# Kernel tuning notes

Measured on AMD Instinct MI355X. Metric: run time of the kernel, lower is better.

The kernel has to match this reference:

```python
import jax, jax.numpy as jnp
import numpy as np

N_HEAD = 16
ROPE_BASE = 10000.0
EPS = 1e-6


def _rms_norm(x):
    return x / jnp.sqrt(jnp.mean(x * x, axis=-1, keepdims=True) + EPS)


def _rotary_cos_sin(n_pos, dim, dtype):
    # NOTE: faithful to the source, n_pos == n_head (not seq_len) because
    # Rotary.forward reads x.shape[2] of a (B,T,H,D) tensor.
    inv_freq = 1.0 / (ROPE_BASE ** (jnp.arange(0, dim, 2, dtype=jnp.float32) / dim))
    t = jnp.arange(n_pos, dtype=jnp.float32)
    freqs = jnp.outer(t, inv_freq)  # (n_pos, dim//2)
    return jnp.cos(freqs).astype(dtype)[None, None], jnp.sin(freqs).astype(dtype)[None, None]


def _apply_rotary(x, cos, sin):
    d = x.shape[-1] // 2
    x1, x2 = x[..., :d], x[..., d:]
    return jnp.concatenate([x1 * cos + x2 * sin, -x1 * sin + x2 * cos], axis=-1)


def setup_inputs() -> dict:
    key = jax.random.key(0)
    ks = jax.random.split(key, 8)
    B, T, C = 4, 1024, 2048
    x = jax.random.normal(ks[0], (B, T, C), dtype=jnp.float32)
    v1 = jax.random.normal(ks[1], (B, T, N_HEAD, C // N_HEAD), dtype=jnp.float32)
    s = 0.02
    W_qkv = jax.random.normal(ks[2], (C, 3 * C), dtype=jnp.float32) * s
    b_qkv = jax.random.normal(ks[3], (3 * C,), dtype=jnp.float32) * s
    W_proj = jax.random.normal(ks[4], (C, C), dtype=jnp.float32) * s
    b_proj = jax.random.normal(ks[5], (C,), dtype=jnp.float32) * s
    lamb = jnp.float32(0.5)
    return {"x": x, "v1": v1, "W_qkv": W_qkv, "b_qkv": b_qkv,
            "W_proj": W_proj, "b_proj": b_proj, "lamb": lamb}


def reference(x, v1, W_qkv, b_qkv, W_proj, b_proj, lamb):
    B, T, C = x.shape
    H = N_HEAD
    D = C // H
    qkv = x @ W_qkv + b_qkv  # (B,T,3C)
    q, k, v = jnp.split(qkv, 3, axis=-1)
    q = q.reshape(B, T, H, D)
    k = k.reshape(B, T, H, D)
    v = v.reshape(B, T, H, D)
    v1 = v1.reshape(B, T, H, D)
    value = (1.0 - lamb) * v + lamb * v1  # lambda value-residual mix
    q = _rms_norm(q)
    k = _rms_norm(k)
    cos, sin = _rotary_cos_sin(H, D, x.dtype)  # rotary over head axis (source bug, kept)
    q = _apply_rotary(q, cos, sin)
    k = _apply_rotary(k, cos, sin)
    # causal attention, default flex_attention scale 1/sqrt(D)
    scale = 1.0 / jnp.sqrt(jnp.float32(D)).astype(x.dtype)
    scores = jnp.einsum('bqhd,bkhd->bhqk', q, k) * scale
    causal = jnp.tril(jnp.ones((T, T), dtype=bool))
    scores = jnp.where(causal[None, None], scores, jnp.finfo(scores.dtype).min)
    probs = jax.nn.softmax(scores, axis=-1)
    attn = jnp.einsum('bhqk,bkhd->bqhd', probs, value).reshape(B, T, C)
    out = attn @ W_proj + b_proj
    return out, v1
```

## Files before the change

### kernel.cpp

```cpp
#include <hip/hip_runtime.h>
#include <stdint.h>
#include <stddef.h>

typedef unsigned short u16;
typedef __attribute__((ext_vector_type(8))) short  bf16x8;
typedef __attribute__((ext_vector_type(4))) unsigned short u16x4;
typedef __attribute__((ext_vector_type(4))) float  f32x4;

#define DEVI __device__ __forceinline__

DEVI float bf2f(u16 u){ union{uint32_t i; float f;} v; v.i = ((uint32_t)u)<<16; return v.f; }
DEVI u16 f2bf(float f){ union{float f; uint32_t i;} v; v.f=f; uint32_t r = v.i + 0x7fffu + ((v.i>>16)&1u); return (u16)(r>>16); }

DEVI void gload_lds16(const void* g, void* l){
  __builtin_amdgcn_global_load_lds((const __attribute__((address_space(1))) void*)g,
                                   (__attribute__((address_space(3))) void*)l, 16, 0, 0);
}

__global__ void k_cvt_bf16(const float* __restrict__ in, u16* __restrict__ out, int n){
  int i = (blockIdx.x*256 + threadIdx.x)*4;
  int st = gridDim.x*256*4;
  for (; i < n; i += st){
    f32x4 v = *(const f32x4*)(in + i);
    u16x4 o;
    #pragma unroll
    for (int j=0;j<4;j++) o[j] = f2bf(v[j]);
    *(u16x4*)(out + i) = o;
  }
}

__global__ __launch_bounds__(256) void k_transpose_cvt(const float* __restrict__ in, u16* __restrict__ out, int K, int N){
  __shared__ float tile[32][33];
  int nb = blockIdx.x*32, kb = blockIdx.y*32;
  int tx = threadIdx.x & 31, ty = threadIdx.x >> 5;
  #pragma unroll
  for (int i=0;i<32;i+=8)
    tile[ty+i][tx] = in[(size_t)(kb+ty+i)*N + nb+tx];
  __syncthreads();
  #pragma unroll
  for (int i=0;i<32;i+=8)
    out[(size_t)(nb+ty+i)*K + kb+tx] = f2bf(tile[tx][ty+i]);
}

#define STG(LP, GP, KH) \
  gload_lds16((GP) + offs[0] + (KH)*32, (LP) + (KH)*8192 + tid*8); \
  gload_lds16((GP) + offs[1] + (KH)*32, (LP) + (KH)*8192 + 4096 + tid*8);

#define RD_A(SP, KH, MH, DST) \
  { _Pragma("unroll") for (int f=0; f<4; f++){ \
      int row_ = wm*128 + (MH)*64 + f*16 + lr; \
      int rp_ = row_>>1; \
      int slot_ = ((((row_&1)<<2) | lg) ^ (rp_&7)); \
      DST[f] = *(const bf16x8*)((const char*)(SP) + (KH)*16384 + rp_*128 + slot_*16); } }

#define RD_B(SP, KH, DST) \
  { _Pragma("unroll") for (int nf=0; nf<4; nf++){ \
      int row_ = wn*64 + nf*16 + lr; \
      int rp_ = row_>>1; \
      int slot_ = ((((row_&1)<<2) | lg) ^ (rp_&7)); \
      DST[nf] = *(const bf16x8*)((const char*)(SP) + (KH)*16384 + rp_*128 + slot_*16); } }

#define MMQ(MH, AA, BB) \
  __builtin_amdgcn_s_setprio(1); \
  { _Pragma("unroll") for (int f=0; f<4; f++) \
    { _Pragma("unroll") for (int nf=0; nf<4; nf++) \
      acc[(MH)*4+f][nf] = __builtin_amdgcn_mfma_f32_16x16x32_bf16(AA[f], BB[nf], acc[(MH)*4+f][nf], 0,0,0); } } \
  __builtin_amdgcn_s_setprio(0);

#define BAR_LGKM \
  __builtin_amdgcn_s_barrier(); \
  __builtin_amdgcn_sched_barrier(0); \
  asm volatile("s_waitcnt lgkmcnt(0)" ::: "memory"); \
  __builtin_amdgcn_sched_barrier(0);

#define WAITV(N) asm volatile("s_waitcnt vmcnt(" #N ")" ::: "memory");
#define ORDER_FENCE __builtin_amdgcn_sched_barrier(0); asm volatile("" ::: "memory");

template<bool OUT_BF16>
__global__ __launch_bounds__(512) void k_gemm256(
    const u16* __restrict__ A, const u16* __restrict__ Bt,
    const float* __restrict__ bias, void* __restrict__ Cout,
    int M, int N, int K, int nbn)
{
  __shared__ __attribute__((aligned(16))) u16 sAm[2][2][8192];
  __shared__ __attribute__((aligned(16))) u16 sBm[2][2][8192];
  int nwg = gridDim.x;
  int orig = blockIdx.x;
  int wgid = (orig & 7)*(nwg>>3) + (orig>>3);
  int bm = wgid / nbn, bn = wgid % nbn;
  const int tid = threadIdx.x;
  const int wid = tid>>6, l = tid&63;
  const int lr = l&15, lg = l>>4;
  const int wm = wid>>2, wn = wid&3;
  const size_t rowA = (size_t)bm*256;
  const size_t rowB = (size_t)bn*256;

  uint32_t offs[2];
  #pragma unroll
  for (int it=0; it<2; it++){
    int cc = it*512 + tid;
    int rp = cc>>3, comb = (cc&7) ^ (rp&7);
    int row = rp*2 + (comb>>2), k16 = comb&3;
    offs[it] = (uint32_t)(row*K + k16*8);
  }
  const u16* Abase = A + rowA*K;
  const u16* Bbase = Bt + rowB*K;

  f32x4 acc[8][4] = {};
  bf16x8 a0[4], a1[4], b0[4], b1[4];
  const int NT = K>>6;

  STG(&sAm[0][0][0], Abase, 0);
  STG(&sBm[0][0][0], Bbase, 0);
  ORDER_FENCE;
  STG(&sAm[0][0][0], Abase, 1);
  STG(&sBm[0][0][0], Bbase, 1);
  WAITV(0);
  __builtin_amdgcn_s_barrier();
  __builtin_amdgcn_sched_barrier(0);

  const u16* An = Abase + 64;
  const u16* Bn = Bbase + 64;
  for (int kt=0; kt<NT-1; ++kt){
    const u16* sAr = &sAm[kt&1][0][0];
    const u16* sBr = &sBm[kt&1][0][0];
    u16* sAw = &sAm[(kt&1)^1][0][0];
    u16* sBw = &sBm[(kt&1)^1][0][0];
    RD_B(sBr, 0, b0);
    RD_A(sAr, 0, 0, a0);
    STG(sAw, An, 0);
    BAR_LGKM;
    MMQ(0, a0, b0);
    RD_A(sAr, 0, 1, a1);
    STG(sBw, Bn, 0);
    WAITV(4);
    BAR_LGKM;
    MMQ(1, a1, b0);
    RD_B(sBr, 1, b1);
    RD_A(sAr, 1, 0, a0);
    STG(sAw, An, 1);
    BAR_LGKM;
    MMQ(0, a0, b1);
    RD_A(sAr, 1, 1, a1);
    STG(sBw, Bn, 1);
    WAITV(4);
    BAR_LGKM;
    MMQ(1, a1, b1);
    An += 64; Bn += 64;
  }
  {
    const u16* sAr = &sAm[(NT-1)&1][0][0];
    const u16* sBr = &sBm[(NT-1)&1][0][0];
    RD_B(sBr, 0, b0);
    RD_A(sAr, 0, 0, a0);
    BAR_LGKM;
    MMQ(0, a0, b0);
    RD_A(sAr, 0, 1, a1);
    WAITV(0);
    BAR_LGKM;
    MMQ(1, a1, b0);
    RD_B(sBr, 1, b1);
    RD_A(sAr, 1, 0, a0);
    BAR_LGKM;
    MMQ(0, a0, b1);
    RD_A(sAr, 1, 1, a1);
    BAR_LGKM;
    MMQ(1, a1, b1);
  }

  #pragma unroll
  for (int nf=0; nf<4; nf++){
    int col = bn*256 + wn*64 + nf*16 + lr;
    float bv = bias[col];
    #pragma unroll
    for (int m=0; m<8; m++){
      #pragma unroll
      for (int j=0; j<4; j++){
        int row = bm*256 + wm*128 + m*16 + lg*4 + j;
        float v = acc[m][nf][j] + bv;
        if (OUT_BF16) ((u16*)Cout)[(size_t)row*N + col] = f2bf(v);
        else          ((float*)Cout)[(size_t)row*N + col] = v;
      }
    }
  }
}

template<bool OUT_BF16>
__global__ __launch_bounds__(256) void k_gemm_bt(
    const u16* __restrict__ A, const u16* __restrict__ Bt,
    const float* __restrict__ bias, void* __restrict__ Cout,
    int M, int N, int K, int nbn)
{
  __shared__ __attribute__((aligned(16))) u16 sA[128*64];
  __shared__ __attribute__((aligned(16))) u16 sB[128*64];
  int nwg = gridDim.x;
  int orig = blockIdx.x;
  int wgid = (orig & 7)*(nwg>>3) + (orig>>3);
  int bm = wgid / nbn, bn = wgid % nbn;
  const int tid = threadIdx.x;
  const int w = tid>>6, l = tid&63;
  const int lr = l&15, lg = l>>4;
  const int wr = (w>>1)*64, wc = (w&1)*64;
  const size_t rowA = (size_t)bm*128;
  const size_t rowB = (size_t)bn*128;
  f32x4 acc[4][4] = {};
  for (int k0=0; k0<K; k0+=64){
    #pragma unroll
    for (int it=0; it<4; ++it){
      int c = it*256 + tid;
      int r = c>>3, k8 = (c&7) ^ (r&7);
      gload_lds16(A + (rowA+r)*K + k0 + k8*8, &sA[c*8]);
    }
    #pragma unroll
    for (int it=0; it<4; ++it){
      int c = it*256 + tid;
      int r = c>>3, k8 = (c&7) ^ (r&7);
      gload_lds16(Bt + (rowB+r)*K + k0 + k8*8, &sB[c*8]);
    }
    __syncthreads();
    #pragma unroll
    for (int ks=0; ks<2; ++ks){
      bf16x8 af[4], bfr[4];
      #pragma unroll
      for (int m=0;m<4;m++){
        int row = wr + m*16 + lr, k = ks*32 + lg*8;
        int byt = ((row<<7) + (k<<1)) ^ ((row&7)<<4);
        af[m] = *(const bf16x8*)((const char*)sA + byt);
      }
      #pragma unroll
      for (int n=0;n<4;n++){
        int row = wc + n*16 + lr, k = ks*32 + lg*8;
        int byt = ((row<<7) + (k<<1)) ^ ((row&7)<<4);
        bfr[n] = *(const bf16x8*)((const char*)sB + byt);
      }
      #pragma unroll
      for (int m=0;m<4;m++)
        #pragma unroll
        for (int n=0;n<4;n++)
          acc[m][n] = __builtin_amdgcn_mfma_f32_16x16x32_bf16(af[m], bfr[n], acc[m][n], 0,0,0);
    }
    __syncthreads();
  }
  #pragma unroll
  for (int n=0;n<4;n++){
    int col = bn*128 + wc + n*16 + lr;
    float bv = bias[col];
    #pragma unroll
    for (int m=0;m<4;m++){
      #pragma unroll
      for (int j=0;j<4;j++){
        int row = bm*128 + wr + m*16 + lg*4 + j;
        float v = acc[m][n][j] + bv;
        if (OUT_BF16) ((u16*)Cout)[(size_t)row*N + col] = f2bf(v);
        else          ((float*)Cout)[(size_t)row*N + col] = v;
      }
    }
  }
}

DEVI void unpack16(const u16* p, float* f){
  bf16x8 a = *(const bf16x8*)p, b = *(const bf16x8*)(p+8);
  #pragma unroll
  for (int i=0;i<8;i++){ f[i]=bf2f((u16)a[i]); f[8+i]=bf2f((u16)b[i]); }
}

__global__ __launch_bounds__(256) void k_qkv_post(
    const u16*  __restrict__ qkv,
    const float* __restrict__ v1,
    const float* __restrict__ lambp,
    u16* __restrict__ qn,
    u16* __restrict__ kn,
    u16* __restrict__ vT,
    float* __restrict__ v1out)
{
  __shared__ float cosv[64], sinv[64];
  __shared__ __attribute__((aligned(16))) u16 sv[64][136];
  int bid = blockIdx.x;
  int tb = bid & 15, h = (bid>>4)&15, b = bid>>8;
  int tid = threadIdx.x;
  if (tid < 64){
    float ang = (float)h * exp2f(-(float)tid * 0.2076205059304595f);
    cosv[tid] = cosf(ang);
    sinv[tid] = sinf(ang);
  }
  float lamb = lambp[0];
  int row = tid>>2, p = tid&3;
  int t = tb*64 + row;
  size_t base = ((size_t)(b*1024 + t))*6144 + (size_t)h*128;
  __syncthreads();

  #pragma unroll
  for (int qc=0; qc<2; ++qc){
    const u16* src = qkv + base + qc*2048;
    u16* dst = (qc==0 ? qn : kn) + ((size_t)(b*1024+t))*2048 + h*128;
    int j0 = p*16;
    float x1[16], x2[16];
    unpack16(src + j0, x1);
    unpack16(src + 64 + j0, x2);
    float ss = 0.f;
    #pragma unroll
    for (int i=0;i<16;i++) ss += x1[i]*x1[i] + x2[i]*x2[i];
    ss += __shfl_xor(ss, 1);
    ss += __shfl_xor(ss, 2);
    float rn = rsqrtf(ss*(1.0f/128.0f) + 1e-6f);
    bf16x8 o1a,o1b,o2a,o2b;
    #pragma unroll
    for (int i=0;i<16;i++){
      float c = cosv[j0+i], s = sinv[j0+i];
      u16 a = f2bf(( x1[i]*c + x2[i]*s)*rn);
      u16 bq= f2bf((-x1[i]*s + x2[i]*c)*rn);
      if (i<8){ o1a[i]=(short)a; o2a[i]=(short)bq; } else { o1b[i-8]=(short)a; o2b[i-8]=(short)bq; }
    }
    *(bf16x8*)(dst + j0)      = o1a;
    *(bf16x8*)(dst + j0 + 8)  = o1b;
    *(bf16x8*)(dst + 64 + j0)     = o2a;
    *(bf16x8*)(dst + 64 + j0 + 8) = o2b;
  }

  {
    const u16* srcv = qkv + base + 4096;
    size_t v1off = (((size_t)(b*1024+t))*16 + h)*128;
    const float* src1 = v1 + v1off;
    float* dst1 = v1out + v1off;
    int d0 = p*32;
    #pragma unroll
    for (int c8=0;c8<4;c8++){
      bf16x8 vv = *(const bf16x8*)(srcv + d0 + c8*8);
      f32x4 a0 = *(const f32x4*)(src1 + d0 + c8*8);
      f32x4 a1 = *(const f32x4*)(src1 + d0 + c8*8 + 4);
      *(f32x4*)(dst1 + d0 + c8*8) = a0;
      *(f32x4*)(dst1 + d0 + c8*8 + 4) = a1;
      bf16x8 o;
      #pragma unroll
      for (int i=0;i<8;i++){
        float x1v = (i<4)? a0[i] : a1[i-4];
        o[i] = (short)f2bf((1.0f-lamb)*bf2f((u16)vv[i]) + lamb*x1v);
      }
      *(bf16x8*)(&sv[row][d0 + c8*8]) = o;
    }
  }
  __syncthreads();
  {
    int d = tid>>1, tc = (tid&1)*32;
    u16 tmp[32];
    #pragma unroll
    for (int i=0;i<32;i++) tmp[i] = sv[tc+i][d];
    u16* dst = vT + (((size_t)(b*16+h))*128 + d)*1024 + tb*64 + tc;
    #pragma unroll
    for (int c8=0;c8<4;c8++){
      bf16x8 o;
      #pragma unroll
      for (int i=0;i<8;i++) o[i]=(short)tmp[c8*8+i];
      *(bf16x8*)(dst + c8*8) = o;
    }
  }
}

__global__ __launch_bounds__(256) void k_attn(
    const u16* __restrict__ Q,
    const u16* __restrict__ Kn,
    const u16* __restrict__ Vt,
    u16* __restrict__ O)
{
  __shared__ __attribute__((aligned(16))) u16 sK[2][64*128];
  __shared__ __attribute__((aligned(16))) u16 sV[2][128*64];
  __shared__ __attribute__((aligned(16))) u16 sP[4][16*64];
  int bid = blockIdx.x;
  int qi = 15 - (bid>>6);
  int bh = bid & 63;
  int h = bh & 15, b = bh >> 4;
  int tid = threadIdx.x, w = tid>>6, l = tid&63, lr = l&15, lg = l>>4;
  int qrow = qi*64 + w*16;
  bf16x8 aq[4];
  {
    const u16* qp = Q + ((size_t)(b*1024 + qrow + lr))*2048 + h*128 + lg*8;
    #pragma unroll
    for (int ks=0; ks<4; ++ks) aq[ks] = *(const bf16x8*)(qp + ks*32);
  }
  f32x4 accO[8] = {};
  float mrun[4], srun[4];
  #pragma unroll
  for (int j=0;j<4;j++){ mrun[j] = -INFINITY; srun[j]=0.f; }
  const float scale = 0.08838834764831845f;
  const size_t kbase = (size_t)(b*1024)*2048 + (size_t)h*128;
  const u16* vbase = Vt + ((size_t)(b*16+h))*128*1024;

  auto STAGE = [&](int kt, int buf){
    #pragma unroll
    for (int it=0; it<4; ++it){
      int c = it*256+tid;
      int key = c>>4, d16 = (c&15)^(key&7);
      gload_lds16(Kn + kbase + (size_t)(kt*64+key)*2048 + d16*8, &sK[buf][c*8]);
    }
    #pragma unroll
    for (int it=0; it<4; ++it){
      int c = it*256+tid;
      int d = c>>3, k8 = (c&7)^(d&7);
      gload_lds16(vbase + (size_t)d*1024 + kt*64 + k8*8, &sV[buf][c*8]);
    }
  };

  STAGE(0, 0);
  int cur = 0;
  for (int kt=0; kt<=qi; ++kt){
    if (kt < qi){
      STAGE(kt+1, cur^1);
      asm volatile("s_waitcnt vmcnt(8)" ::: "memory");
    } else {
      asm volatile("s_waitcnt vmcnt(0)" ::: "memory");
    }
    __builtin_amdgcn_s_barrier();
    __builtin_amdgcn_sched_barrier(0);
    const char* kb = (const char*)sK[cur];
    const char* vb = (const char*)sV[cur];

    f32x4 accS[4] = {};
    __builtin_amdgcn_s_setprio(1);
    #pragma unroll
    for (int ks=0; ks<4; ++ks){
      #pragma unroll
      for (int n=0;n<4;n++){
        int key = n*16+lr, k = ks*32+lg*8;
        int byt = ((key<<8) + (k<<1)) ^ ((key&7)<<4);
        bf16x8 bk = *(const bf16x8*)(kb + byt);
        accS[n] = __builtin_amdgcn_mfma_f32_16x16x32_bf16(aq[ks], bk, accS[n], 0,0,0);
      }
    }
    __builtin_amdgcn_s_setprio(0);
    bool diag = (kt == qi);
    float pj[4][4];
    #pragma unroll
    for (int j=0;j<4;j++){
      int qg = qrow + lg*4 + j;
      float mx = -INFINITY;
      #pragma unroll
      for (int n=0;n<4;n++){
        float s = accS[n][j]*scale;
        if (diag && (kt*64 + n*16 + lr) > qg) s = -1e30f;
        pj[n][j] = s;
        mx = fmaxf(mx, s);
      }
      #pragma unroll
      for (int off=1; off<16; off<<=1) mx = fmaxf(mx, __shfl_xor(mx, off));
      float mnew = fmaxf(mrun[j], mx);
      float fac = __expf(mrun[j] - mnew);
      float ps = 0.f;
      #pragma unroll
      for (int n=0;n<4;n++){ float e = __expf(pj[n][j]-mnew); pj[n][j]=e; ps += e; }
      #pragma unroll
      for (int off=1; off<16; off<<=1) ps += __shfl_xor(ps, off);
      srun[j] = srun[j]*fac + ps;
      mrun[j] = mnew;
      #pragma unroll
      for (int n=0;n<8;n++) accO[n][j] *= fac;
    }
    #pragma unroll
    for (int n=0;n<4;n++)
      #pragma unroll
      for (int j=0;j<4;j++){
        int q = lg*4+j, key = n*16+lr;
        int byt = ((q<<7) + (key<<1)) ^ ((q&7)<<4);
        *(u16*)((char*)sP[w] + byt) = f2bf(pj[n][j]);
      }
    bf16x8 pA[2];
    #pragma unroll
    for (int ks=0; ks<2; ++ks){
      int k = ks*32 + lg*8;
      int byt = ((lr<<7) + (k<<1)) ^ ((lr&7)<<4);
      pA[ks] = *(const bf16x8*)((const char*)sP[w] + byt);
    }
    __builtin_amdgcn_s_setprio(1);
    #pragma unroll
    for (int ks=0; ks<2; ++ks)
      #pragma unroll
      for (int n=0;n<8;n++){
        int d = n*16+lr, k = ks*32+lg*8;
        int byt = ((d<<7) + (k<<1)) ^ ((d&7)<<4);
        bf16x8 bv = *(const bf16x8*)(vb + byt);
        accO[n] = __builtin_amdgcn_mfma_f32_16x16x32_bf16(pA[ks], bv, accO[n], 0,0,0);
      }
    __builtin_amdgcn_s_setprio(0);
    __builtin_amdgcn_s_barrier();
    cur ^= 1;
  }
  #pragma unroll
  for (int j=0;j<4;j++){
    float inv = 1.0f / srun[j];
    int row = qrow + lg*4 + j;
    u16* op = O + ((size_t)(b*1024+row))*2048 + h*128;
    #pragma unroll
    for (int n=0;n<8;n++)
      op[n*16+lr] = f2bf(accO[n][j]*inv);
  }
}

extern "C" void kernel_launch(void* const* d_in, const int* in_sizes, int n_in,
                              void* d_out, int out_size, void* d_ws, size_t ws_size,
                              hipStream_t stream)
{
  const float* x     = (const float*)d_in[0];
  const float* v1    = (const float*)d_in[1];
  const float* Wqkv  = (const float*)d_in[2];
  const float* bqkv  = (const float*)d_in[3];
  const float* Wproj = (const float*)d_in[4];
  const float* bproj = (const float*)d_in[5];
  const float* lamb  = (const float*)d_in[6];

  char* ws = (char*)d_ws;
  u16* qkv_b  = (u16*)(ws);
  u16* WqkvT  = (u16*)(ws +  50331648);
  u16* WprojT = (u16*)(ws +  75497472);
  u16* xb     = (u16*)(ws +  83886080);
  u16* vT     = xb;
  u16* qn     = (u16*)(ws + 100663296);
  u16* kn     = (u16*)(ws + 117440512);
  u16* attn_b = qkv_b;

  float* out = (float*)d_out;

  hipLaunchKernelGGL(k_cvt_bf16, dim3(2048), dim3(256), 0, stream, x, xb, 8388608);
  hipLaunchKernelGGL(k_transpose_cvt, dim3(192, 64), dim3(256), 0, stream, Wqkv,  WqkvT,  2048, 6144);
  hipLaunchKernelGGL(k_transpose_cvt, dim3(64, 64),  dim3(256), 0, stream, Wproj, WprojT, 2048, 2048);
  hipLaunchKernelGGL((k_gemm256<true>), dim3(384), dim3(512), 0, stream, xb, WqkvT, bqkv, (void*)qkv_b, 4096, 6144, 2048, 24);
  hipLaunchKernelGGL(k_qkv_post, dim3(1024), dim3(256), 0, stream, qkv_b, v1, lamb, qn, kn, vT, out + 8388608);
  hipLaunchKernelGGL(k_attn, dim3(1024), dim3(256), 0, stream, qn, kn, vT, attn_b);
  hipLaunchKernelGGL((k_gemm_bt<false>), dim3(32*16), dim3(256), 0, stream, attn_b, WprojT, bproj, (void*)out, 4096, 2048, 2048, 16);
}
```

Measured before the change: 289.6 us.

## Deepen GEMM LDS pipeline to a rolling slab ring with more loads in flight

Reworks the 256x256 GEMM main loop so that shared memory is treated as four 32-wide K slabs per operand, used as a ring rather than a double buffer of 64-wide tiles. The prologue issues loads for three slabs ahead, and each unrolled 128-K iteration refills a slab as soon as it has been consumed, waiting on vmcnt(8) instead of draining to fewer outstanding loads. The aim is to hide global-load latency behind the MFMA work by keeping more global-to-LDS transfers in flight. The price is more complex vmcnt bookkeeping and a requirement that K be a multiple of 128, and a wrong wait count could give a race.

```diff
diff --git a/kernel.cpp b/kernel.cpp
--- a/kernel.cpp
+++ b/kernel.cpp
@@ -42,29 +42,29 @@
     out[(size_t)(nb+ty+i)*K + kb+tx] = f2bf(tile[tx][ty+i]);
 }
 
-#define STG(LP, GP, KH) \
-  gload_lds16((GP) + offs[0] + (KH)*32, (LP) + (KH)*8192 + tid*8); \
-  gload_lds16((GP) + offs[1] + (KH)*32, (LP) + (KH)*8192 + 4096 + tid*8);
-
-#define RD_A(SP, KH, MH, DST) \
+#define STG2(SLAB, GSRC) \
+  gload_lds16((GSRC) + offs[0], (SLAB) + tid*8); \
+  gload_lds16((GSRC) + offs[1], (SLAB) + 4096 + tid*8);
+
+#define RD_Am(SLAB, MQ, DST) \
   { _Pragma("unroll") for (int f=0; f<4; f++){ \
-      int row_ = wm*128 + (MH)*64 + f*16 + lr; \
+      int row_ = wm*128 + (MQ)*64 + f*16 + lr; \
       int rp_ = row_>>1; \
       int slot_ = ((((row_&1)<<2) | lg) ^ (rp_&7)); \
-      DST[f] = *(const bf16x8*)((const char*)(SP) + (KH)*16384 + rp_*128 + slot_*16); } }
-
-#define RD_B(SP, KH, DST) \
+      DST[f] = *(const bf16x8*)((const char*)(SLAB) + rp_*128 + slot_*16); } }
+
+#define RD_Bm(SLAB, DST) \
   { _Pragma("unroll") for (int nf=0; nf<4; nf++){ \
       int row_ = wn*64 + nf*16 + lr; \
       int rp_ = row_>>1; \
       int slot_ = ((((row_&1)<<2) | lg) ^ (rp_&7)); \
-      DST[nf] = *(const bf16x8*)((const char*)(SP) + (KH)*16384 + rp_*128 + slot_*16); } }
-
-#define MMQ(MH, AA, BB) \
+      DST[nf] = *(const bf16x8*)((const char*)(SLAB) + rp_*128 + slot_*16); } }
+
+#define MMQ(MQ, AA, BB) \
   __builtin_amdgcn_s_setprio(1); \
   { _Pragma("unroll") for (int f=0; f<4; f++) \
     { _Pragma("unroll") for (int nf=0; nf<4; nf++) \
-      acc[(MH)*4+f][nf] = __builtin_amdgcn_mfma_f32_16x16x32_bf16(AA[f], BB[nf], acc[(MH)*4+f][nf], 0,0,0); } } \
+      acc[(MQ)*4+f][nf] = __builtin_amdgcn_mfma_f32_16x16x32_bf16(AA[f], BB[nf], acc[(MQ)*4+f][nf], 0,0,0); } } \
   __builtin_amdgcn_s_setprio(0);
 
 #define BAR_LGKM \
@@ -82,8 +82,8 @@
     const float* __restrict__ bias, void* __restrict__ Cout,
     int M, int N, int K, int nbn)
 {
-  __shared__ __attribute__((aligned(16))) u16 sAm[2][2][8192];
-  __shared__ __attribute__((aligned(16))) u16 sBm[2][2][8192];
+  __shared__ __attribute__((aligned(16))) u16 sA[2][2][8192];
+  __shared__ __attribute__((aligned(16))) u16 sB[2][2][8192];
   int nwg = gridDim.x;
   int orig = blockIdx.x;
   int wgid = (orig & 7)*(nwg>>3) + (orig>>3);
@@ -103,69 +103,52 @@
     int row = rp*2 + (comb>>2), k16 = comb&3;
     offs[it] = (uint32_t)(row*K + k16*8);
   }
-  const u16* Abase = A + rowA*K;
-  const u16* Bbase = Bt + rowB*K;
+  const u16* Ab = A + rowA*K;
+  const u16* Bb = Bt + rowB*K;
 
   f32x4 acc[8][4] = {};
   bf16x8 a0[4], a1[4], b0[4], b1[4];
-  const int NT = K>>6;
-
-  STG(&sAm[0][0][0], Abase, 0);
-  STG(&sBm[0][0][0], Bbase, 0);
-  ORDER_FENCE;
-  STG(&sAm[0][0][0], Abase, 1);
-  STG(&sBm[0][0][0], Bbase, 1);
-  WAITV(0);
+  const int NI = K>>7;
+
+  STG2(&sB[0][0][0], Bb);       ORDER_FENCE;
+  STG2(&sA[0][0][0], Ab);       ORDER_FENCE;
+  STG2(&sB[0][1][0], Bb+32);    ORDER_FENCE;
+  STG2(&sA[0][1][0], Ab+32);    ORDER_FENCE;
+  STG2(&sB[1][0][0], Bb+64);    ORDER_FENCE;
+  STG2(&sA[1][0][0], Ab+64);
+  WAITV(8);
   __builtin_amdgcn_s_barrier();
   __builtin_amdgcn_sched_barrier(0);
 
-  const u16* An = Abase + 64;
-  const u16* Bn = Bbase + 64;
-  for (int kt=0; kt<NT-1; ++kt){
-    const u16* sAr = &sAm[kt&1][0][0];
-    const u16* sBr = &sBm[kt&1][0][0];
-    u16* sAw = &sAm[(kt&1)^1][0][0];
-    u16* sBw = &sBm[(kt&1)^1][0][0];
-    RD_B(sBr, 0, b0);
-    RD_A(sAr, 0, 0, a0);
-    STG(sAw, An, 0);
-    BAR_LGKM;
-    MMQ(0, a0, b0);
-    RD_A(sAr, 0, 1, a1);
-    STG(sBw, Bn, 0);
-    WAITV(4);
-    BAR_LGKM;
-    MMQ(1, a1, b0);
-    RD_B(sBr, 1, b1);
-    RD_A(sAr, 1, 0, a0);
-    STG(sAw, An, 1);
-    BAR_LGKM;
-    MMQ(0, a0, b1);
-    RD_A(sAr, 1, 1, a1);
-    STG(sBw, Bn, 1);
-    WAITV(4);
-    BAR_LGKM;
-    MMQ(1, a1, b1);
-    An += 64; Bn += 64;
-  }
-  {
-    const u16* sAr = &sAm[(NT-1)&1][0][0];
-    const u16* sBr = &sBm[(NT-1)&1][0][0];
-    RD_B(sBr, 0, b0);
-    RD_A(sAr, 0, 0, a0);
-    BAR_LGKM;
-    MMQ(0, a0, b0);
-    RD_A(sAr, 0, 1, a1);
-    WAITV(0);
-    BAR_LGKM;
-    MMQ(1, a1, b0);
-    RD_B(sBr, 1, b1);
-    RD_A(sAr, 1, 0, a0);
-    BAR_LGKM;
-    MMQ(0, a0, b1);
-    RD_A(sAr, 1, 1, a1);
-    BAR_LGKM;
-    MMQ(1, a1, b1);
+  for (int it=0; it<NI; ++it){
+    const bool last = (it == NI-1);
+    const u16* Ai = Ab + it*128;
+    const u16* Bi = Bb + it*128;
+    RD_Bm(&sB[0][0][0], b0); RD_Am(&sA[0][0][0], 0, a0);
+    STG2(&sB[1][1][0], Bi+96);
+    BAR_LGKM; MMQ(0, a0, b0);
+    RD_Am(&sA[0][0][0], 1, a1);
+    STG2(&sA[1][1][0], Ai+96);
+    WAITV(8);
+    BAR_LGKM; MMQ(1, a1, b0);
+    RD_Bm(&sB[0][1][0], b1); RD_Am(&sA[0][1][0], 0, a0);
+    if (!last){ STG2(&sB[0][0][0], Bi+128); }
+    BAR_LGKM; MMQ(0, a0, b1);
+    RD_Am(&sA[0][1][0], 1, a1);
+    if (!last){ STG2(&sA[0][0][0], Ai+128); WAITV(8); } else { WAITV(4); }
+    BAR_LGKM; MMQ(1, a1, b1);
+    RD_Bm(&sB[1][0][0], b0); RD_Am(&sA[1][0][0], 0, a0);
+    if (!last){ STG2(&sB[0][1][0], Bi+160); }
+    BAR_LGKM; MMQ(0, a0, b0);
+    RD_Am(&sA[1][0][0], 1, a1);
+    if (!last){ STG2(&sA[0][1][0], Ai+160); WAITV(8); } else { WAITV(0); }
+    BAR_LGKM; MMQ(1, a1, b0);
+    RD_Bm(&sB[1][1][0], b1); RD_Am(&sA[1][1][0], 0, a0);
+    if (!last){ STG2(&sB[1][0][0], Bi+192); }
+    BAR_LGKM; MMQ(0, a0, b1);
+    RD_Am(&sA[1][1][0], 1, a1);
+    if (!last){ STG2(&sA[1][0][0], Ai+192); WAITV(8); }
+    BAR_LGKM; MMQ(1, a1, b1);
   }
 
   #pragma unroll
```

Result: no change. 292.0 us (+0.8%).
